# Optimization experiments

Hardware: AMD Instinct MI355X
Metric: run time of the kernel (lower is better)

The kernel has to match this reference:

```python
import jax, jax.numpy as jnp
import numpy as np
from jax import lax

B, S, F, H, A, C = 256, 128, 128, 512, 512, 128


def _gru_cell(x, h, Wih, Whh, bih, bhh):
    # PyTorch GRU cell: gates ordered (r, z, n)
    gi = x @ Wih.T + bih            # [B, 3H]
    gh = h @ Whh.T + bhh            # [B, 3H]
    ir, iz, inn = jnp.split(gi, 3, axis=-1)
    hr, hz, hn = jnp.split(gh, 3, axis=-1)
    r = jax.nn.sigmoid(ir + hr)
    z = jax.nn.sigmoid(iz + hz)
    n = jnp.tanh(inn + r * hn)
    return (1.0 - z) * n + z * h


def setup_inputs() -> dict:
    key = jax.random.key(0)
    ks = jax.random.split(key, 13)
    def n(k, shape, s=0.05):
        return jax.random.normal(k, shape, dtype=jnp.float32) * s
    return dict(
        x=n(ks[0], (B, S, F), 1.0),
        y=jax.random.randint(ks[1], (B, C), 0, S),
        enc_Wih=n(ks[2], (3 * H, F)), enc_Whh=n(ks[3], (3 * H, H)),
        enc_bih=n(ks[4], (3 * H,)), enc_bhh=n(ks[5], (3 * H,)),
        dec_Wih=n(ks[6], (3 * H, F)), dec_Whh=n(ks[7], (3 * H, H)),
        dec_bih=n(ks[8], (3 * H,)), dec_bhh=n(ks[9], (3 * H,)),
        w1=n(ks[10], (A, H)), w2=n(ks[11], (A, H)), v=n(ks[12], (A,)),
    )


def reference(x, y, enc_Wih, enc_Whh, enc_bih, enc_bhh,
              dec_Wih, dec_Whh, dec_bih, dec_bhh, w1, w2, v):
    b, s, f = x.shape
    c = y.shape[1]
    h0 = jnp.zeros((b, H), x.dtype)

    # ---- encoder GRU over sequence ----
    def enc_step(h, xt):
        h2 = _gru_cell(xt, h, enc_Wih, enc_Whh, enc_bih, enc_bhh)
        return h2, h2
    hT, enc_out = lax.scan(enc_step, h0, jnp.swapaxes(x, 0, 1))  # enc_out [S,B,H]
    enc_out = jnp.swapaxes(enc_out, 0, 1)                        # [B,S,H]

    # w1(enc_out) is loop-invariant: precompute (same math as recomputing per step)
    enc_proj = jnp.einsum('bsh,ah->bsa', enc_out, w1)            # [B,S,A]

    # ---- decoder pointer loop (teacher_force_ratio=0.0 -> always use argmax) ----
    def dec_step(carry, y_i):
        h, dec_in = carry
        h = _gru_cell(dec_in, h, dec_Wih, dec_Whh, dec_bih, dec_bhh)  # [B,H]
        att = jax.nn.relu(enc_proj + (h @ w2.T)[:, None, :])          # [B,S,A]
        prob = jax.nn.softmax(jnp.einsum('bsa,a->bs', att, v), axis=1)  # [B,S]
        # faithful to original: F.cross_entropy applied to probabilities
        logp = jax.nn.log_softmax(prob, axis=1)
        step_loss = -jnp.mean(jnp.take_along_axis(logp, y_i[:, None], axis=1))
        pred = jnp.argmax(prob, axis=1)                               # [B]
        dec_in_next = jnp.take_along_axis(x, pred[:, None, None], axis=1)[:, 0, :]
        return (h, dec_in_next), (pred, step_loss)

    dec_in0 = jnp.zeros((b, f), x.dtype)
    (_, _), (preds, losses) = lax.scan(dec_step, (hT, dec_in0), y.T)
    preds = preds.T                                   # [B, C]
    loss = jnp.sum(losses) / b / c
    return preds, loss
```

## Files before the change

### kernel.cpp

```cpp
#include <hip/hip_runtime.h>
#include <math.h>

#define B_ 256
#define S_ 128
#define F_ 128
#define H_ 512
#define A_ 512
#define C_ 128

#define DOT4(va, vb) ((va).x*(vb).x + (va).y*(vb).y + (va).z*(vb).z + (va).w*(vb).w)

__global__ __launch_bounds__(256)
void transpose_x(const float* __restrict__ x, float* __restrict__ xT)
{
    const int t = blockIdx.x >> 2;
    const int f0 = (blockIdx.x & 3) * 32;
    const int b = threadIdx.x;
#pragma unroll 4
    for (int ff = 0; ff < 32; ++ff) {
        int f = f0 + ff;
        xT[(size_t)t * (F_ * B_) + (size_t)f * B_ + b] =
            x[(size_t)b * (S_ * F_) + (size_t)t * F_ + f];
    }
}

__global__ __launch_bounds__(256)
void prep_w6(const float* __restrict__ Wih, const float* __restrict__ Whh,
             float* __restrict__ W6)
{
    int id = blockIdx.x * 256 + threadIdx.x;
    if (id >= 256 * 640 * 6) return;
    int up = id / 3840;
    int rem = id - up * 3840;
    int k = rem / 6, g = rem - k * 6;
    int row = (g >> 1) * H_ + up * 2 + (g & 1);
    float val;
    if (k < F_) val = Wih[(size_t)row * F_ + k];
    else        val = Whh[(size_t)row * H_ + (k - F_)];
    W6[id] = val;
}

__global__ __launch_bounds__(256)
void prep_w2q(const float* __restrict__ w2, float4* __restrict__ w2q,
              float* __restrict__ dec_inT)
{
    int id = blockIdx.x * 256 + threadIdx.x;
    if (id < 128 * 512) {
        int k4 = id >> 9, a = id & 511;
        const float* s = w2 + (size_t)a * H_ + k4 * 4;
        w2q[id] = make_float4(s[0], s[1], s[2], s[3]);
    }
    if (id < F_ * B_) dec_inT[id] = 0.f;
}

__global__ __launch_bounds__(256)
void prep_bias(const float* __restrict__ ebih, const float* __restrict__ ebhh,
               const float* __restrict__ dbih, const float* __restrict__ dbhh,
               float* __restrict__ bias4e, float* __restrict__ bias4d,
               float* __restrict__ h0T, int* __restrict__ flags)
{
    int id = blockIdx.x * 256 + threadIdx.x;
    if (id < H_ * B_) h0T[id] = 0.f;
    if (id < S_) flags[id] = 0;
    if (id < H_) {
        bias4e[id * 4 + 0] = ebih[id] + ebhh[id];
        bias4e[id * 4 + 1] = ebih[H_ + id] + ebhh[H_ + id];
        bias4e[id * 4 + 2] = ebih[2 * H_ + id];
        bias4e[id * 4 + 3] = ebhh[2 * H_ + id];
        bias4d[id * 4 + 0] = dbih[id] + dbhh[id];
        bias4d[id * 4 + 1] = dbih[H_ + id] + dbhh[H_ + id];
        bias4d[id * 4 + 2] = dbih[2 * H_ + id];
        bias4d[id * 4 + 3] = dbhh[2 * H_ + id];
    }
}

template<int NH>
__device__ __forceinline__ void acc_range(const float* __restrict__ src,
                                          const float* __restrict__ W6k,
                                          int nk, int b, float* __restrict__ acc)
{
    float a0[8], a1[8];
#pragma unroll
    for (int j = 0; j < 8; ++j) a0[j] = src[(size_t)j * B_ + b];
    for (int kc = 0; kc < nk; kc += 8) {
        if (kc + 8 < nk) {
#pragma unroll
            for (int j = 0; j < 8; ++j) a1[j] = src[(size_t)(kc + 8 + j) * B_ + b];
        }
        const float* Wr = W6k + (size_t)kc * 6;
#pragma unroll
        for (int j = 0; j < 8; ++j) {
            float av = a0[j];
            acc[0]      = fmaf(av, Wr[j * 6 + 0], acc[0]);
            acc[1]      = fmaf(av, Wr[j * 6 + 1], acc[1]);
            acc[2]      = fmaf(av, Wr[j * 6 + 2], acc[2]);
            acc[3]      = fmaf(av, Wr[j * 6 + 3], acc[3]);
            acc[NH]     = fmaf(av, Wr[j * 6 + 4], acc[NH]);
            acc[NH + 1] = fmaf(av, Wr[j * 6 + 5], acc[NH + 1]);
        }
#pragma unroll
        for (int j = 0; j < 8; ++j) a0[j] = a1[j];
    }
}

__global__ __launch_bounds__(512)
void enc_persist(const float* __restrict__ xT,
                 const float* __restrict__ W6,
                 const float* __restrict__ bias4,
                 const float* __restrict__ h0T,
                 float* __restrict__ encT,
                 int* __restrict__ flags)
{
    __shared__ float accL[256][6];
    const int tid = threadIdx.x;
    const int lane = tid & 63;
    const int w = tid >> 6;
    const int bg = w & 3;
    const int kw = w >> 2;
    const int b = bg * 64 + lane;
    const int up = blockIdx.x;
    const float* Wb = W6 + (size_t)up * (640 * 6);
    const int u0 = up * 2, u1 = u0 + 1;
    const float4 bb0 = *(const float4*)(bias4 + u0 * 4);
    const float4 bb1 = *(const float4*)(bias4 + u1 * 4);

    for (int t = 0; t < S_; ++t) {
        const float* inT = xT + (size_t)t * (F_ * B_);
        const float* hinT = (t == 0) ? h0T : encT + (size_t)(t - 1) * (H_ * B_);
        float* houtT = encT + (size_t)t * (H_ * B_);

        float acc[8];
#pragma unroll
        for (int g = 0; g < 8; ++g) acc[g] = 0.f;

        if (kw == 0) acc_range<4>(inT, Wb, F_, b, acc);

        if (t > 0) {
            if (tid == 0) {
                while (__hip_atomic_load(&flags[t - 1], __ATOMIC_RELAXED,
                                         __HIP_MEMORY_SCOPE_AGENT) != 256) {
                    __builtin_amdgcn_s_sleep(1);
                }
            }
        }
        __syncthreads();

        if (kw == 0) {
            acc_range<6>(hinT, Wb + F_ * 6, 192, b, acc);
        } else {
            acc_range<6>(hinT + (size_t)192 * B_, Wb + 320 * 6, 320, b, acc);
        }

        if (kw == 1) {
            const int li = tid & 255;
            accL[li][0] = acc[0]; accL[li][1] = acc[1];
            accL[li][2] = acc[2]; accL[li][3] = acc[3];
            accL[li][4] = acc[6]; accL[li][5] = acc[7];
        }
        __syncthreads();
        if (kw == 0) {
            float rr0 = 1.f / (1.f + expf(-(acc[0] + accL[tid][0] + bb0.x)));
            float rr1 = 1.f / (1.f + expf(-(acc[1] + accL[tid][1] + bb1.x)));
            float zz0 = 1.f / (1.f + expf(-(acc[2] + accL[tid][2] + bb0.y)));
            float zz1 = 1.f / (1.f + expf(-(acc[3] + accL[tid][3] + bb1.y)));
            float hn0 = acc[6] + accL[tid][4] + bb0.w;
            float hn1 = acc[7] + accL[tid][5] + bb1.w;
            float nn0 = tanhf(acc[4] + bb0.z + rr0 * hn0);
            float nn1 = tanhf(acc[5] + bb1.z + rr1 * hn1);
            float ho0 = hinT[(size_t)u0 * B_ + b];
            float ho1 = hinT[(size_t)u1 * B_ + b];
            float h0v = (1.f - zz0) * nn0 + zz0 * ho0;
            float h1v = (1.f - zz1) * nn1 + zz1 * ho1;
            __hip_atomic_store(&houtT[(size_t)u0 * B_ + b], h0v,
                               __ATOMIC_RELAXED, __HIP_MEMORY_SCOPE_AGENT);
            __hip_atomic_store(&houtT[(size_t)u1 * B_ + b], h1v,
                               __ATOMIC_RELAXED, __HIP_MEMORY_SCOPE_AGENT);
        }
        asm volatile("s_waitcnt vmcnt(0)" ::: "memory");
        __syncthreads();
        if (tid == 0) {
            __hip_atomic_fetch_add(&flags[t], 1, __ATOMIC_RELAXED,
                                   __HIP_MEMORY_SCOPE_AGENT);
        }
    }
}

__global__ __launch_bounds__(512)
void gru_step(const float* __restrict__ inT,
              const float* __restrict__ hinT,
              const float* __restrict__ W6,
              const float* __restrict__ bias4,
              float* __restrict__ houtT,
              float* __restrict__ hB)
{
    __shared__ float accL[256][6];
    const int tid = threadIdx.x;
    const int lane = tid & 63;
    const int w = tid >> 6;
    const int bg = w & 3;
    const int kw = w >> 2;
    const int b = bg * 64 + lane;
    const int up = blockIdx.x;
    const float* Wb = W6 + (size_t)up * (640 * 6);

    float acc[8];
#pragma unroll
    for (int g = 0; g < 8; ++g) acc[g] = 0.f;

    if (kw == 0) {
        acc_range<4>(inT, Wb, F_, b, acc);
        acc_range<6>(hinT, Wb + F_ * 6, 192, b, acc);
    } else {
        acc_range<6>(hinT + (size_t)192 * B_, Wb + 320 * 6, 320, b, acc);
    }

    if (kw == 1) {
        const int li = tid & 255;
        accL[li][0] = acc[0]; accL[li][1] = acc[1];
        accL[li][2] = acc[2]; accL[li][3] = acc[3];
        accL[li][4] = acc[6]; accL[li][5] = acc[7];
    }
    __syncthreads();
    if (kw == 0) {
        const int u0 = up * 2, u1 = u0 + 1;
        float4 bb0 = *(const float4*)(bias4 + u0 * 4);
        float4 bb1 = *(const float4*)(bias4 + u1 * 4);
        float rr0 = 1.f / (1.f + expf(-(acc[0] + accL[tid][0] + bb0.x)));
        float rr1 = 1.f / (1.f + expf(-(acc[1] + accL[tid][1] + bb1.x)));
        float zz0 = 1.f / (1.f + expf(-(acc[2] + accL[tid][2] + bb0.y)));
        float zz1 = 1.f / (1.f + expf(-(acc[3] + accL[tid][3] + bb1.y)));
        float hn0 = acc[6] + accL[tid][4] + bb0.w;
        float hn1 = acc[7] + accL[tid][5] + bb1.w;
        float nn0 = tanhf(acc[4] + bb0.z + rr0 * hn0);
        float nn1 = tanhf(acc[5] + bb1.z + rr1 * hn1);
        float ho0 = hinT[(size_t)u0 * B_ + b];
        float ho1 = hinT[(size_t)u1 * B_ + b];
        float h0v = (1.f - zz0) * nn0 + zz0 * ho0;
        float h1v = (1.f - zz1) * nn1 + zz1 * ho1;
        houtT[(size_t)u0 * B_ + b] = h0v;
        houtT[(size_t)u1 * B_ + b] = h1v;
        if (hB) {
            hB[(size_t)b * H_ + u0] = h0v;
            hB[(size_t)b * H_ + u1] = h1v;
        }
    }
}

__global__ __launch_bounds__(512)
void w2attn_step(const float* __restrict__ hB,
                 const float4* __restrict__ w2q,
                 const float* __restrict__ v, const int* __restrict__ y,
                 int step, const float* __restrict__ x,
                 const float* __restrict__ proj,
                 float* __restrict__ dec_inT,
                 float* __restrict__ nlogp, float* __restrict__ preds_out)
{
    const int b = blockIdx.x;
    const int tid = threadIdx.x;
    __shared__ float sh[512];
    __shared__ float sq[512];
    __shared__ float sScore[S_], sProb[S_];
    __shared__ int sPred;

    sh[tid] = hB[(size_t)b * H_ + tid];
    __syncthreads();

    {
        float acc = 0.f;
        const float4* wp = w2q + tid;
#pragma unroll 8
        for (int k4 = 0; k4 < 128; ++k4) {
            float4 hv = *(const float4*)&sh[k4 * 4];
            float4 wv4 = wp[(size_t)k4 * 512];
            acc += DOT4(hv, wv4);
        }
        sq[tid] = acc;
    }
    __syncthreads();

    const int wv = tid >> 6, ln = tid & 63;
    float4 q0 = *(const float4*)&sq[ln * 8];
    float4 q1 = *(const float4*)&sq[ln * 8 + 4];
    float4 v0r = *(const float4*)(v + ln * 8);
    float4 v1r = *(const float4*)(v + ln * 8 + 4);
    const float* epb = proj + (size_t)b * (S_ * A_);
    for (int si = 0; si < 16; ++si) {
        int s = si * 8 + wv;
        const float* row = epb + (size_t)s * A_ + ln * 8;
        float4 p0 = *(const float4*)(row);
        float4 p1 = *(const float4*)(row + 4);
        float acc = fmaxf(p0.x + q0.x, 0.f) * v0r.x
                  + fmaxf(p0.y + q0.y, 0.f) * v0r.y
                  + fmaxf(p0.z + q0.z, 0.f) * v0r.z
                  + fmaxf(p0.w + q0.w, 0.f) * v0r.w
                  + fmaxf(p1.x + q1.x, 0.f) * v1r.x
                  + fmaxf(p1.y + q1.y, 0.f) * v1r.y
                  + fmaxf(p1.z + q1.z, 0.f) * v1r.z
                  + fmaxf(p1.w + q1.w, 0.f) * v1r.w;
#pragma unroll
        for (int off = 32; off; off >>= 1) acc += __shfl_down(acc, off);
        if (ln == 0) sScore[s] = acc;
    }
    __syncthreads();

    if (tid < 64) {
        float s0v = sScore[tid], s1v = sScore[tid + 64];
        float m = fmaxf(s0v, s1v);
#pragma unroll
        for (int off = 32; off; off >>= 1) m = fmaxf(m, __shfl_xor(m, off));
        float e0 = expf(s0v - m), e1 = expf(s1v - m);
        float se = e0 + e1;
#pragma unroll
        for (int off = 32; off; off >>= 1) se += __shfl_xor(se, off);
        float p0 = e0 / se, p1 = e1 / se;
        sProb[tid] = p0; sProb[tid + 64] = p1;
        float pm = fmaxf(p0, p1);
#pragma unroll
        for (int off = 32; off; off >>= 1) pm = fmaxf(pm, __shfl_xor(pm, off));
        float t0 = expf(p0 - pm), t1 = expf(p1 - pm);
        float T = t0 + t1;
#pragma unroll
        for (int off = 32; off; off >>= 1) T += __shfl_xor(T, off);
        float bv = p0; int bi2 = tid;
        if (p1 > bv) { bv = p1; bi2 = tid + 64; }
#pragma unroll
        for (int off = 32; off; off >>= 1) {
            float ov = __shfl_xor(bv, off);
            int oi = __shfl_xor(bi2, off);
            if (ov > bv || (ov == bv && oi < bi2)) { bv = ov; bi2 = oi; }
        }
        if (tid == 0) {
            sPred = bi2;
            int yy = y[(size_t)b * C_ + step];
            float py = sProb[yy];
            nlogp[(size_t)step * B_ + b] = -(py - pm - logf(T));
            preds_out[(size_t)b * C_ + step] = (float)bi2;
        }
    }
    __syncthreads();

    const int pred = sPred;
    if (tid < F_) {
        dec_inT[(size_t)tid * B_ + b] = x[((size_t)b * S_ + pred) * F_ + tid];
    }
}

__global__ __launch_bounds__(256)
void proj_gemm(const float* __restrict__ encT, const float* __restrict__ w1,
               float* __restrict__ proj)
{
    __shared__ float sA[32][128];
    __shared__ float sB[32][128];
    const int tid = threadIdx.x;
    const int s = blockIdx.z;
    const int b0 = blockIdx.y * 128;
    const int a0 = blockIdx.x * 128;
    const int tx = tid & 15, ty = tid >> 4;

    float acc[8][8];
#pragma unroll
    for (int i = 0; i < 8; ++i)
#pragma unroll
        for (int j = 0; j < 8; ++j) acc[i][j] = 0.f;

    const float* Abase = encT + (size_t)s * (H_ * B_) + b0;
    for (int kc = 0; kc < H_; kc += 32) {
#pragma unroll
        for (int p = 0; p < 16; ++p) {
            int idx = tid + p * 256;
            int kj = idx >> 7, bb = idx & 127;
            sA[kj][bb] = Abase[(size_t)(kc + kj) * B_ + bb];
        }
#pragma unroll
        for (int p = 0; p < 16; ++p) {
            int idx = tid + p * 256;
            int aa = idx >> 5, kj = idx & 31;
            sB[kj][aa] = w1[(size_t)(a0 + aa) * H_ + kc + kj];
        }
        __syncthreads();
#pragma unroll
        for (int kj = 0; kj < 32; ++kj) {
            float4 af0 = *(const float4*)&sA[kj][ty * 8];
            float4 af1 = *(const float4*)&sA[kj][ty * 8 + 4];
            float4 bf0 = *(const float4*)&sB[kj][tx * 8];
            float4 bf1 = *(const float4*)&sB[kj][tx * 8 + 4];
            float am[8] = {af0.x, af0.y, af0.z, af0.w, af1.x, af1.y, af1.z, af1.w};
            float bn[8] = {bf0.x, bf0.y, bf0.z, bf0.w, bf1.x, bf1.y, bf1.z, bf1.w};
#pragma unroll
            for (int i = 0; i < 8; ++i)
#pragma unroll
                for (int j = 0; j < 8; ++j)
                    acc[i][j] = fmaf(am[i], bn[j], acc[i][j]);
        }
        __syncthreads();
    }
#pragma unroll
    for (int i = 0; i < 8; ++i) {
        float* dst = proj + ((size_t)(b0 + ty * 8 + i) * S_ + s) * A_ + a0 + tx * 8;
        *(float4*)(dst) = make_float4(acc[i][0], acc[i][1], acc[i][2], acc[i][3]);
        *(float4*)(dst + 4) = make_float4(acc[i][4], acc[i][5], acc[i][6], acc[i][7]);
    }
}

__global__ void final_loss(const float* __restrict__ nlogp, float* __restrict__ out)
{
    __shared__ float part[C_];
    const int i = threadIdx.x;
    float s = 0.f;
    for (int b = 0; b < B_; ++b) s += nlogp[(size_t)i * B_ + b];
    part[i] = s / (float)B_;
    __syncthreads();
    if (i == 0) {
        float t = 0.f;
        for (int k = 0; k < C_; ++k) t += part[k];
        out[0] = t / (float)B_ / (float)C_;
    }
}

extern "C" void kernel_launch(void* const* d_in, const int* in_sizes, int n_in,
                              void* d_out, int out_size, void* d_ws, size_t ws_size,
                              hipStream_t stream)
{
    (void)in_sizes; (void)n_in; (void)out_size; (void)ws_size;
    const float* x    = (const float*)d_in[0];
    const int*   y    = (const int*)d_in[1];
    const float* eWih = (const float*)d_in[2];
    const float* eWhh = (const float*)d_in[3];
    const float* ebih = (const float*)d_in[4];
    const float* ebhh = (const float*)d_in[5];
    const float* dWih = (const float*)d_in[6];
    const float* dWhh = (const float*)d_in[7];
    const float* dbih = (const float*)d_in[8];
    const float* dbhh = (const float*)d_in[9];
    const float* w1   = (const float*)d_in[10];
    const float* w2   = (const float*)d_in[11];
    const float* v    = (const float*)d_in[12];
    float* out = (float*)d_out;

    float* ws = (float*)d_ws;
    float* encT    = ws;
    float* W6d     = ws;
    float* w2qf    = ws + 983040;
    float* hT0     = ws + 1245184;
    float* hT1     = ws + 1376256;
    float* dec_inT = ws + 1507328;
    float* nlogp   = ws + 1540096;
    float* hB      = ws + 1572864;
    float* encT127 = ws + 16646144;
    float* projB   = ws + 16777216;
    float* xT      = projB;
    float* W6e     = projB + 4194304;
    float* h0T     = projB + 5177344;
    float* bias4e  = ws + 33554432;
    float* bias4d  = ws + 33554432 + 2048;
    int*   flags   = (int*)(ws + 33554432 + 4096);

    prep_bias<<<dim3(512), 256, 0, stream>>>(ebih, ebhh, dbih, dbhh,
                                             bias4e, bias4d, h0T, flags);
    transpose_x<<<dim3(512), 256, 0, stream>>>(x, xT);
    prep_w6<<<dim3(3840), 256, 0, stream>>>(eWih, eWhh, W6e);

    {
        void* a[] = { (void*)&xT, (void*)&W6e, (void*)&bias4e, (void*)&h0T,
                      (void*)&encT, (void*)&flags };
        hipLaunchCooperativeKernel((const void*)enc_persist,
                                   dim3(256), dim3(512), a, 0, stream);
    }

    proj_gemm<<<dim3(4, 2, 128), 256, 0, stream>>>(encT, w1, projB);

    prep_w6<<<dim3(3840), 256, 0, stream>>>(dWih, dWhh, W6d);
    prep_w2q<<<dim3(256), 256, 0, stream>>>(w2, (float4*)w2qf, dec_inT);

    float* hb[2] = { hT0, hT1 };
    for (int i = 0; i < C_; ++i) {
        const float* hin = (i == 0) ? encT127 : hb[(i & 1) ^ 1];
        float* hout = hb[i & 1];
        gru_step<<<dim3(256), 512, 0, stream>>>(dec_inT, hin, W6d, bias4d,
                                                hout, hB);
        w2attn_step<<<dim3(256), 512, 0, stream>>>(hB, (const float4*)w2qf, v, y,
                                                   i, x, projB, dec_inT,
                                                   nlogp, out);
    }

    final_loss<<<dim3(1), 128, 0, stream>>>(nlogp, out + (size_t)B_ * C_);
}
```

Measured before the change: 8.790 ms.

## Fuse decoder GRU and attention kernels with a flag-based grid barrier

Merges the per-step decoder GRU kernel and the attention/argmax kernel into one kernel per step. A spin barrier on per-block padded flags now separates the GRU phase from the attention phase, replacing a kernel boundary. The encoder's single shared atomic counter per timestep is also replaced by per-block progress flags that 64 threads poll together, which cuts atomic contention. The decoder launch is not cooperative, so the barrier assumes all 256 blocks are resident at once, which is a risk.

```diff
diff --git a/kernel.cpp b/kernel.cpp
--- a/kernel.cpp
+++ b/kernel.cpp
@@ -57,11 +57,12 @@
 void prep_bias(const float* __restrict__ ebih, const float* __restrict__ ebhh,
                const float* __restrict__ dbih, const float* __restrict__ dbhh,
                float* __restrict__ bias4e, float* __restrict__ bias4d,
-               float* __restrict__ h0T, int* __restrict__ flags)
+               float* __restrict__ h0T, int* __restrict__ eflags,
+               int* __restrict__ dflags)
 {
     int id = blockIdx.x * 256 + threadIdx.x;
     if (id < H_ * B_) h0T[id] = 0.f;
-    if (id < S_) flags[id] = 0;
+    if (id < 256 * 32) { eflags[id] = 0; dflags[id] = 0; }
     if (id < H_) {
         bias4e[id * 4 + 0] = ebih[id] + ebhh[id];
         bias4e[id * 4 + 1] = ebih[H_ + id] + ebhh[H_ + id];
@@ -103,13 +104,32 @@
     }
 }
 
+__device__ __forceinline__ void wait_all_blocks(const int* __restrict__ flags,
+                                                int tid, int target)
+{
+    if (tid < 64) {
+        while (true) {
+            int mn = 0x7fffffff;
+#pragma unroll
+            for (int q = 0; q < 4; ++q) {
+                int vq = __hip_atomic_load(&flags[(tid + q * 64) * 32],
+                                           __ATOMIC_RELAXED,
+                                           __HIP_MEMORY_SCOPE_AGENT);
+                mn = vq < mn ? vq : mn;
+            }
+            if (__all(mn >= target)) break;
+            __builtin_amdgcn_s_sleep(2);
+        }
+    }
+}
+
 __global__ __launch_bounds__(512)
 void enc_persist(const float* __restrict__ xT,
                  const float* __restrict__ W6,
                  const float* __restrict__ bias4,
                  const float* __restrict__ h0T,
                  float* __restrict__ encT,
-                 int* __restrict__ flags)
+                 int* __restrict__ eflags)
 {
     __shared__ float accL[256][6];
     const int tid = threadIdx.x;
@@ -135,14 +155,7 @@
 
         if (kw == 0) acc_range<4>(inT, Wb, F_, b, acc);
 
-        if (t > 0) {
-            if (tid == 0) {
-                while (__hip_atomic_load(&flags[t - 1], __ATOMIC_RELAXED,
-                                         __HIP_MEMORY_SCOPE_AGENT) != 256) {
-                    __builtin_amdgcn_s_sleep(1);
-                }
-            }
-        }
+        if (t > 0) wait_all_blocks(eflags, tid, t);
         __syncthreads();
 
         if (kw == 0) {
@@ -179,21 +192,33 @@
         asm volatile("s_waitcnt vmcnt(0)" ::: "memory");
         __syncthreads();
         if (tid == 0) {
-            __hip_atomic_fetch_add(&flags[t], 1, __ATOMIC_RELAXED,
-                                   __HIP_MEMORY_SCOPE_AGENT);
+            __hip_atomic_store(&eflags[up * 32], t + 1,
+                               __ATOMIC_RELAXED, __HIP_MEMORY_SCOPE_AGENT);
         }
     }
 }
 
 __global__ __launch_bounds__(512)
-void gru_step(const float* __restrict__ inT,
-              const float* __restrict__ hinT,
-              const float* __restrict__ W6,
-              const float* __restrict__ bias4,
-              float* __restrict__ houtT,
-              float* __restrict__ hB)
+void dec_fused(const float* __restrict__ dec_in,
+               const float* __restrict__ hinT,
+               const float* __restrict__ W6,
+               const float* __restrict__ bias4,
+               float* __restrict__ houtT,
+               float* __restrict__ hB,
+               const float4* __restrict__ w2q,
+               const float* __restrict__ v, const int* __restrict__ y,
+               int step, const float* __restrict__ x,
+               const float* __restrict__ proj,
+               float* __restrict__ dec_out,
+               float* __restrict__ nlogp, float* __restrict__ preds_out,
+               int* __restrict__ dflags)
 {
     __shared__ float accL[256][6];
+    __shared__ float sh[512];
+    __shared__ float sq[512];
+    __shared__ float sScore[S_], sProb[S_];
+    __shared__ int sPred;
+
     const int tid = threadIdx.x;
     const int lane = tid & 63;
     const int w = tid >> 6;
@@ -201,68 +226,64 @@
     const int kw = w >> 2;
     const int b = bg * 64 + lane;
     const int up = blockIdx.x;
-    const float* Wb = W6 + (size_t)up * (640 * 6);
-
-    float acc[8];
-#pragma unroll
-    for (int g = 0; g < 8; ++g) acc[g] = 0.f;
-
-    if (kw == 0) {
-        acc_range<4>(inT, Wb, F_, b, acc);
-        acc_range<6>(hinT, Wb + F_ * 6, 192, b, acc);
-    } else {
-        acc_range<6>(hinT + (size_t)192 * B_, Wb + 320 * 6, 320, b, acc);
-    }
-
-    if (kw == 1) {
-        const int li = tid & 255;
-        accL[li][0] = acc[0]; accL[li][1] = acc[1];
-        accL[li][2] = acc[2]; accL[li][3] = acc[3];
-        accL[li][4] = acc[6]; accL[li][5] = acc[7];
-    }
+
+    {
+        const float* Wb = W6 + (size_t)up * (640 * 6);
+        float acc[8];
+#pragma unroll
+        for (int g = 0; g < 8; ++g) acc[g] = 0.f;
+
+        if (kw == 0) {
+            acc_range<4>(dec_in, Wb, F_, b, acc);
+            acc_range<6>(hinT, Wb + F_ * 6, 192, b, acc);
+        } else {
+            acc_range<6>(hinT + (size_t)192 * B_, Wb + 320 * 6, 320, b, acc);
+        }
+
+        if (kw == 1) {
+            const int li = tid & 255;
+            accL[li][0] = acc[0]; accL[li][1] = acc[1];
+            accL[li][2] = acc[2]; accL[li][3] = acc[3];
+            accL[li][4] = acc[6]; accL[li][5] = acc[7];
+        }
+        __syncthreads();
+        if (kw == 0) {
+            const int u0 = up * 2, u1 = u0 + 1;
+            float4 bb0 = *(const float4*)(bias4 + u0 * 4);
+            float4 bb1 = *(const float4*)(bias4 + u1 * 4);
+            float rr0 = 1.f / (1.f + expf(-(acc[0] + accL[tid][0] + bb0.x)));
+            float rr1 = 1.f / (1.f + expf(-(acc[1] + accL[tid][1] + bb1.x)));
+            float zz0 = 1.f / (1.f + expf(-(acc[2] + accL[tid][2] + bb0.y)));
+            float zz1 = 1.f / (1.f + expf(-(acc[3] + accL[tid][3] + bb1.y)));
+            float hn0 = acc[6] + accL[tid][4] + bb0.w;
+            float hn1 = acc[7] + accL[tid][5] + bb1.w;
+            float nn0 = tanhf(acc[4] + bb0.z + rr0 * hn0);
+            float nn1 = tanhf(acc[5] + bb1.z + rr1 * hn1);
+            float ho0 = hinT[(size_t)u0 * B_ + b];
+            float ho1 = hinT[(size_t)u1 * B_ + b];
+            float h0v = (1.f - zz0) * nn0 + zz0 * ho0;
+            float h1v = (1.f - zz1) * nn1 + zz1 * ho1;
+            houtT[(size_t)u0 * B_ + b] = h0v;
+            houtT[(size_t)u1 * B_ + b] = h1v;
+            __hip_atomic_store(&hB[(size_t)b * H_ + u0], h0v,
+                               __ATOMIC_RELAXED, __HIP_MEMORY_SCOPE_AGENT);
+            __hip_atomic_store(&hB[(size_t)b * H_ + u1], h1v,
+                               __ATOMIC_RELAXED, __HIP_MEMORY_SCOPE_AGENT);
+        }
+        asm volatile("s_waitcnt vmcnt(0)" ::: "memory");
+        __syncthreads();
+        if (tid == 0) {
+            __hip_atomic_store(&dflags[up * 32], step + 1,
+                               __ATOMIC_RELAXED, __HIP_MEMORY_SCOPE_AGENT);
+        }
+    }
+
+    wait_all_blocks(dflags, tid, step + 1);
     __syncthreads();
-    if (kw == 0) {
-        const int u0 = up * 2, u1 = u0 + 1;
-        float4 bb0 = *(const float4*)(bias4 + u0 * 4);
-        float4 bb1 = *(const float4*)(bias4 + u1 * 4);
-        float rr0 = 1.f / (1.f + expf(-(acc[0] + accL[tid][0] + bb0.x)));
-        float rr1 = 1.f / (1.f + expf(-(acc[1] + accL[tid][1] + bb1.x)));
-        float zz0 = 1.f / (1.f + expf(-(acc[2] + accL[tid][2] + bb0.y)));
-        float zz1 = 1.f / (1.f + expf(-(acc[3] + accL[tid][3] + bb1.y)));
-        float hn0 = acc[6] + accL[tid][4] + bb0.w;
-        float hn1 = acc[7] + accL[tid][5] + bb1.w;
-        float nn0 = tanhf(acc[4] + bb0.z + rr0 * hn0);
-        float nn1 = tanhf(acc[5] + bb1.z + rr1 * hn1);
-        float ho0 = hinT[(size_t)u0 * B_ + b];
-        float ho1 = hinT[(size_t)u1 * B_ + b];
-        float h0v = (1.f - zz0) * nn0 + zz0 * ho0;
-        float h1v = (1.f - zz1) * nn1 + zz1 * ho1;
-        houtT[(size_t)u0 * B_ + b] = h0v;
-        houtT[(size_t)u1 * B_ + b] = h1v;
-        if (hB) {
-            hB[(size_t)b * H_ + u0] = h0v;
-            hB[(size_t)b * H_ + u1] = h1v;
-        }
-    }
-}
-
-__global__ __launch_bounds__(512)
-void w2attn_step(const float* __restrict__ hB,
-                 const float4* __restrict__ w2q,
-                 const float* __restrict__ v, const int* __restrict__ y,
-                 int step, const float* __restrict__ x,
-                 const float* __restrict__ proj,
-                 float* __restrict__ dec_inT,
-                 float* __restrict__ nlogp, float* __restrict__ preds_out)
-{
-    const int b = blockIdx.x;
-    const int tid = threadIdx.x;
-    __shared__ float sh[512];
-    __shared__ float sq[512];
-    __shared__ float sScore[S_], sProb[S_];
-    __shared__ int sPred;
-
-    sh[tid] = hB[(size_t)b * H_ + tid];
+
+    const int bb = blockIdx.x;
+    sh[tid] = __hip_atomic_load(&hB[(size_t)bb * H_ + tid],
+                                __ATOMIC_RELAXED, __HIP_MEMORY_SCOPE_AGENT);
     __syncthreads();
 
     {
@@ -283,7 +304,7 @@
     float4 q1 = *(const float4*)&sq[ln * 8 + 4];
     float4 v0r = *(const float4*)(v + ln * 8);
     float4 v1r = *(const float4*)(v + ln * 8 + 4);
-    const float* epb = proj + (size_t)b * (S_ * A_);
+    const float* epb = proj + (size_t)bb * (S_ * A_);
     for (int si = 0; si < 16; ++si) {
         int s = si * 8 + wv;
         const float* row = epb + (size_t)s * A_ + ln * 8;
@@ -331,17 +352,17 @@
         }
         if (tid == 0) {
             sPred = bi2;
-            int yy = y[(size_t)b * C_ + step];
+            int yy = y[(size_t)bb * C_ + step];
             float py = sProb[yy];
-            nlogp[(size_t)step * B_ + b] = -(py - pm - logf(T));
-            preds_out[(size_t)b * C_ + step] = (float)bi2;
+            nlogp[(size_t)step * B_ + bb] = -(py - pm - logf(T));
+            preds_out[(size_t)bb * C_ + step] = (float)bi2;
         }
     }
     __syncthreads();
 
     const int pred = sPred;
     if (tid < F_) {
-        dec_inT[(size_t)tid * B_ + b] = x[((size_t)b * S_ + pred) * F_ + tid];
+        dec_out[(size_t)tid * B_ + bb] = x[((size_t)bb * S_ + pred) * F_ + tid];
     }
 }
 
@@ -368,8 +389,8 @@
 #pragma unroll
         for (int p = 0; p < 16; ++p) {
             int idx = tid + p * 256;
-            int kj = idx >> 7, bb = idx & 127;
-            sA[kj][bb] = Abase[(size_t)(kc + kj) * B_ + bb];
+            int kj = idx >> 7, bbb = idx & 127;
+            sA[kj][bbb] = Abase[(size_t)(kc + kj) * B_ + bbb];
         }
 #pragma unroll
         for (int p = 0; p < 16; ++p) {
@@ -452,17 +473,18 @@
     float* W6e     = projB + 4194304;
     float* h0T     = projB + 5177344;
     float* bias4e  = ws + 33554432;
-    float* bias4d  = ws + 33554432 + 2048;
-    int*   flags   = (int*)(ws + 33554432 + 4096);
+    float* bias4d  = bias4e + 2048;
+    int*   eflags  = (int*)(bias4d + 2048);
+    int*   dflags  = eflags + 256 * 32;
 
     prep_bias<<<dim3(512), 256, 0, stream>>>(ebih, ebhh, dbih, dbhh,
-                                             bias4e, bias4d, h0T, flags);
+                                             bias4e, bias4d, h0T, eflags, dflags);
     transpose_x<<<dim3(512), 256, 0, stream>>>(x, xT);
     prep_w6<<<dim3(3840), 256, 0, stream>>>(eWih, eWhh, W6e);
 
     {
         void* a[] = { (void*)&xT, (void*)&W6e, (void*)&bias4e, (void*)&h0T,
-                      (void*)&encT, (void*)&flags };
+                      (void*)&encT, (void*)&eflags };
         hipLaunchCooperativeKernel((const void*)enc_persist,
                                    dim3(256), dim3(512), a, 0, stream);
     }
@@ -476,11 +498,9 @@
     for (int i = 0; i < C_; ++i) {
         const float* hin = (i == 0) ? encT127 : hb[(i & 1) ^ 1];
         float* hout = hb[i & 1];
-        gru_step<<<dim3(256), 512, 0, stream>>>(dec_inT, hin, W6d, bias4d,
-                                                hout, hB);
-        w2attn_step<<<dim3(256), 512, 0, stream>>>(hB, (const float4*)w2qf, v, y,
-                                                   i, x, projB, dec_inT,
-                                                   nlogp, out);
+        dec_fused<<<dim3(256), 512, 0, stream>>>(
+            dec_inT, hin, W6d, bias4d, hout, hB, (const float4*)w2qf, v, y,
+            i, x, projB, dec_inT, nlogp, out, dflags);
     }
 
     final_loss<<<dim3(1), 128, 0, stream>>>(nlogp, out + (size_t)B_ * C_);
```

Result: no change. 8.785 ms (-0.1%).
